# Kernel tuning notes

Measured on AMD Instinct MI355X. Metric: run time of the kernel, lower is better.

## Reference

```python
import jax, jax.numpy as jnp
import numpy as np

SR = 44100.0
MIN_GAIN, MAX_GAIN = -48.0, 12.0
MIN_EQ, MAX_EQ = -15.0, 15.0
MIN_CTS, MAX_CTS = -20.0, 10.0
# Freeverb (JUCE Reverb, as used by pedalboard.Reverb) tunings @ 44.1 kHz
COMB_T = [1116, 1188, 1277, 1356, 1422, 1491, 1557, 1617]
AP_T = [556, 441, 341, 225]
COMB_OFF = [0]
for _L in COMB_T:
    COMB_OFF.append(COMB_OFF[-1] + _L)
AP_OFF = [0]
for _L in AP_T:
    AP_OFF.append(AP_OFF[-1] + _L)


def restore(x, lo, hi):
    # inverse of normalize-to-(0,1)
    return x * (hi - lo) + lo


def first_order(fc, kind):
    # bilinear-transform 1st-order HP/LP (pedalboard High/LowpassFilter are 1st order)
    K = jnp.tan(np.pi * fc / SR)
    a1 = (K - 1.0) / (K + 1.0)
    z = jnp.zeros_like(fc)
    if kind == "hp":
        b0 = 1.0 / (1.0 + K)
        b = jnp.stack([b0, -b0, z], -1)
    else:
        b0 = K / (1.0 + K)
        b = jnp.stack([b0, b0, z], -1)
    a = jnp.stack([jnp.ones_like(fc), a1, z], -1)
    return b, a


def shelf(fc, gain_db, high):
    # RBJ cookbook shelf, Q = 1/sqrt(2)
    A = 10.0 ** (gain_db / 40.0)
    w = 2.0 * np.pi * fc / SR
    cw = jnp.cos(w)
    alpha = jnp.sin(w) * (np.sqrt(2.0) / 2.0)
    sq = 2.0 * jnp.sqrt(A) * alpha
    s = 1.0 if high else -1.0
    b0 = A * ((A + 1.0) + s * (A - 1.0) * cw + sq)
    b1 = -2.0 * s * A * ((A - 1.0) + s * (A + 1.0) * cw)
    b2 = A * ((A + 1.0) + s * (A - 1.0) * cw - sq)
    a0 = (A + 1.0) - s * (A - 1.0) * cw + sq
    a1 = 2.0 * s * ((A - 1.0) - s * (A + 1.0) * cw)
    a2 = (A + 1.0) - s * (A - 1.0) * cw - sq
    return jnp.stack([b0, b1, b2], -1), jnp.stack([a0, a1, a2], -1)


def peak(fc, gain_db, q):
    # RBJ cookbook peaking EQ
    A = 10.0 ** (gain_db / 40.0)
    w = 2.0 * np.pi * fc / SR
    cw = jnp.cos(w)
    alpha = jnp.sin(w) / (2.0 * q)
    b = jnp.stack([1.0 + alpha * A, -2.0 * cw, 1.0 - alpha * A], -1)
    a = jnp.stack([1.0 + alpha / A, -2.0 * cw, 1.0 - alpha / A], -1)
    return b, a


def cascade_biquads(x, B, A):
    # x: [N, T]; B, A: [N, 6, 3]. DF2T cascade of 6 sections via one scan.
    B = B / A[..., :1]
    A = A / A[..., :1]
    n_sec = B.shape[1]

    def step(z, xt):  # z: [N, 6, 2], xt: [N]
        s = xt
        zn = []
        for k in range(n_sec):
            y = B[:, k, 0] * s + z[:, k, 0]
            z1 = B[:, k, 1] * s - A[:, k, 1] * y + z[:, k, 1]
            z2 = B[:, k, 2] * s - A[:, k, 2] * y
            zn.append(jnp.stack([z1, z2], -1))
            s = y
        return jnp.stack(zn, 1), s

    z0 = jnp.zeros((x.shape[0], n_sec, 2), x.dtype)
    _, y = jax.lax.scan(step, z0, x.T)
    return y.T


def compressor(x, thr_db, ratio, att_ms, rel_ms):
    # feed-forward compressor, dB-domain gain computer + one-pole attack/release
    a_att = jnp.exp(-1.0 / (att_ms * 1e-3 * SR))  # [N]
    a_rel = jnp.exp(-1.0 / (rel_ms * 1e-3 * SR))
    lvl = 20.0 * jnp.log10(jnp.abs(x) + 1e-6)  # [N, T]
    tgt = jnp.minimum(0.0, (thr_db[:, None] - lvl) * (1.0 - 1.0 / ratio[:, None]))

    def step(g, t):  # g, t: [N] gain reduction in dB (<= 0)
        coef = jnp.where(t < g, a_att, a_rel)
        g = coef * g + (1.0 - coef) * t
        return g, g

    _, g = jax.lax.scan(step, jnp.zeros(x.shape[0], x.dtype), tgt.T)
    return x * 10.0 ** (g.T / 20.0)


def freeverb(x, room, damp01, wet, dry, width):
    # JUCE/Freeverb mono: 8 parallel damped combs -> 4 series allpasses
    fb = room * 0.28 + 0.7
    damp = damp01 * 0.4
    wet1 = 3.0 * wet * 0.5 * (1.0 + width)
    dryg = 2.0 * dry
    N = x.shape[0]
    CL, AL = COMB_OFF[-1], AP_OFF[-1]

    def step(carry, xt):
        cb, ab, st, t = carry
        inp = xt * 0.015
        acc = jnp.zeros_like(xt)
        st_new = []
        for k in range(8):
            idx = COMB_OFF[k] + t % COMB_T[k]
            out = cb[:, idx]
            s = out * (1.0 - damp) + st[:, k] * damp
            cb = cb.at[:, idx].set(inp + s * fb)
            st_new.append(s)
            acc = acc + out
        for k in range(4):
            idx = AP_OFF[k] + t % AP_T[k]
            buf = ab[:, idx]
            ab = ab.at[:, idx].set(acc + buf * 0.5)
            acc = buf - acc
        y = acc * wet1 + xt * dryg
        return (cb, ab, jnp.stack(st_new, 1), t + 1), y

    carry0 = (jnp.zeros((N, CL), x.dtype), jnp.zeros((N, AL), x.dtype),
              jnp.zeros((N, 8), x.dtype), jnp.int32(0))
    _, y = jax.lax.scan(step, carry0, x.T)
    return y.T


def _forward(x, p):
    bs, nt, T = x.shape
    N = bs * nt
    xf = x.reshape(N, T)
    pf = p.reshape(N, 24)

    gain_in = restore(pf[:, 0], MIN_GAIN, MAX_GAIN)
    xf = xf * (10.0 ** (gain_in / 20.0))[:, None]

    hp_fc = restore(pf[:, 1], 0.0, 350.0)
    lp_fc = restore(pf[:, 2], 3000.0, 22000.0)
    hs_fc = restore(pf[:, 3], 1500.0, 16000.0)
    hs_g = restore(pf[:, 4], MIN_EQ, MAX_EQ)
    ls_fc = restore(pf[:, 5], 30.0, 450.0)
    ls_g = restore(pf[:, 6], MIN_EQ, MAX_EQ)
    mh_fc = restore(pf[:, 7], 600.0, 7000.0)
    mh_g = restore(pf[:, 8], MIN_EQ, MAX_EQ)
    mh_q = restore(pf[:, 9], 0.5, 3.0)
    ml_fc = restore(pf[:, 10], 200.0, 2500.0)
    ml_g = restore(pf[:, 11], MIN_EQ, MAX_EQ)
    ml_q = restore(pf[:, 12], 0.5, 3.0)
    c_thr = restore(pf[:, 13], MIN_CTS, MAX_CTS)
    c_rat = restore(pf[:, 14], 1.0, 20.0)
    c_att = restore(pf[:, 15], 1.0, 30.0)
    c_rel = restore(pf[:, 16], 100.0, 4000.0)

    coefs = [first_order(hp_fc, "hp"), first_order(lp_fc, "lp"),
             shelf(hs_fc, hs_g, True), shelf(ls_fc, ls_g, False),
             peak(mh_fc, mh_g, mh_q), peak(ml_fc, ml_g, ml_q)]
    B = jnp.stack([c[0] for c in coefs], 1)  # [N, 6, 3]
    A = jnp.stack([c[1] for c in coefs], 1)
    xf = cascade_biquads(xf, B, A)
    xf = compressor(xf, c_thr, c_rat, c_att, c_rel)
    xf = freeverb(xf, pf[:, 17], pf[:, 18], pf[:, 19], pf[:, 20], pf[:, 21])

    gain_out = restore(pf[:, 22], MIN_GAIN, MAX_GAIN)
    xf = xf * (10.0 ** (gain_out / 20.0))[:, None]

    pan = restore(pf[:, 23], 0.3, 0.7)
    theta = pan * (np.pi / 2.0)
    pang = jnp.stack([jnp.cos(theta), jnp.sin(theta)], -1).reshape(bs, nt, 2)
    y = jnp.einsum("bnt,bnc->bct", xf.reshape(bs, nt, T), pang)

    p_out = jnp.stack([gain_in, hp_fc, lp_fc, hs_fc, hs_g, ls_fc, ls_g,
                       mh_fc, mh_g, mh_q, ml_fc, ml_g, ml_q,
                       c_thr, c_rat, c_att, c_rel,
                       pf[:, 17], pf[:, 18], pf[:, 19], pf[:, 20], pf[:, 21],
                       gain_out, pan], -1).reshape(bs, nt, 24)
    return y, p_out


_forward_jit = jax.jit(_forward)


def setup_inputs() -> dict:
    key = jax.random.key(0)
    k1, k2 = jax.random.split(key)
    x = 0.1 * jax.random.normal(k1, (4, 8, 65536), dtype=jnp.float32)
    p = jax.random.uniform(k2, (4, 8, 24), dtype=jnp.float32)
    return {"x": x, "p": p}


def reference(x, p):
    return _forward_jit(x, p)
```

## Files before the change

kernel.cpp:

```cpp
#include <hip/hip_runtime.h>
#include <math.h>

#define T 65536
#define NCH 32
#define LCHUNK 512
#define CCHUNK 128
#define SB 256
#define NBLK 256

#define OFS_A  0
#define OFS_B1 2097152
#define OFS_I  4194304
#define OFS_P  7340032
#define OFS_M  7342080
#define OFS_V  7346688
#define OFS_Z  7395840


__device__ void norm_store(double b0,double b1,double b2,double a0,double a1,double a2,
                           double* B, double* A1, double* A2, int k){
  B[k*3+0]=b0/a0; B[k*3+1]=b1/a0; B[k*3+2]=b2/a0; A1[k]=a1/a0; A2[k]=a2/a0;
}

__device__ void shelf_coefs(double fc, double g, double s, double* B, double* A1, double* A2, int k){
  double A  = pow(10.0, g/40.0);
  double w  = 2.0*3.14159265358979323846*fc/44100.0;
  double cw = cos(w);
  double al = sin(w)*0.70710678118654752;
  double sq = 2.0*sqrt(A)*al;
  double b0 = A*((A+1.0) + s*(A-1.0)*cw + sq);
  double b1 = -2.0*s*A*((A-1.0) + s*(A+1.0)*cw);
  double b2 = A*((A+1.0) + s*(A-1.0)*cw - sq);
  double a0 = (A+1.0) - s*(A-1.0)*cw + sq;
  double a1 = 2.0*s*((A-1.0) - s*(A+1.0)*cw);
  double a2 = (A+1.0) - s*(A-1.0)*cw - sq;
  norm_store(b0,b1,b2,a0,a1,a2,B,A1,A2,k);
}

__device__ void peak_coefs(double fc, double g, double q, double* B, double* A1, double* A2, int k){
  double A  = pow(10.0, g/40.0);
  double w  = 2.0*3.14159265358979323846*fc/44100.0;
  double cw = cos(w);
  double al = sin(w)/(2.0*q);
  norm_store(1.0+al*A, -2.0*cw, 1.0-al*A, 1.0+al/A, -2.0*cw, 1.0-al/A, B,A1,A2,k);
}

__global__ void k_params(const float* __restrict__ p, float* __restrict__ ws, float* __restrict__ pout){
  int ch = threadIdx.x;
  if (ch >= NCH) return;
  const float* pf = p + ch*24;
  float f[24];
  #pragma unroll
  for (int j=0;j<24;j++) f[j]=pf[j];

  double gain_in = (double)f[0]*60.0 - 48.0;
  double hp_fc  = (double)f[1]*350.0;
  double lp_fc  = (double)f[2]*19000.0 + 3000.0;
  double hs_fc  = (double)f[3]*14500.0 + 1500.0;
  double hs_g   = (double)f[4]*30.0 - 15.0;
  double ls_fc  = (double)f[5]*420.0 + 30.0;
  double ls_g   = (double)f[6]*30.0 - 15.0;
  double mh_fc  = (double)f[7]*6400.0 + 600.0;
  double mh_g   = (double)f[8]*30.0 - 15.0;
  double mh_q   = (double)f[9]*2.5 + 0.5;
  double ml_fc  = (double)f[10]*2300.0 + 200.0;
  double ml_g   = (double)f[11]*30.0 - 15.0;
  double ml_q   = (double)f[12]*2.5 + 0.5;
  double c_thr  = (double)f[13]*30.0 - 20.0;
  double c_rat  = (double)f[14]*19.0 + 1.0;
  double c_att  = (double)f[15]*29.0 + 1.0;
  double c_rel  = (double)f[16]*3900.0 + 100.0;
  double gain_out=(double)f[22]*60.0 - 48.0;
  double pan    = (double)f[23]*0.4 + 0.3;

  double B[18], A1[6], A2[6];
  { double K = tan(3.14159265358979323846*hp_fc/44100.0);
    double a1=(K-1.0)/(K+1.0), b0=1.0/(1.0+K);
    B[0]=b0; B[1]=-b0; B[2]=0.0; A1[0]=a1; A2[0]=0.0; }
  { double K = tan(3.14159265358979323846*lp_fc/44100.0);
    double a1=(K-1.0)/(K+1.0), b0=K/(1.0+K);
    B[3]=b0; B[4]=b0; B[5]=0.0; A1[1]=a1; A2[1]=0.0; }
  shelf_coefs(hs_fc, hs_g,  1.0, B, A1, A2, 2);
  shelf_coefs(ls_fc, ls_g, -1.0, B, A1, A2, 3);
  peak_coefs (mh_fc, mh_g, mh_q, B, A1, A2, 4);
  peak_coefs (ml_fc, ml_g, ml_q, B, A1, A2, 5);

  double gin = pow(10.0, gain_in/20.0);
  B[0]*=gin; B[1]*=gin; B[2]*=gin;

  float* Pc = ws + OFS_P + ch*64;
  #pragma unroll
  for (int k=0;k<6;k++){
    Pc[k]    = (float)B[k*3+0];
    Pc[6+k]  = (float)B[k*3+1];
    Pc[12+k] = (float)B[k*3+2];
    Pc[18+k] = (float)A1[k];
    Pc[24+k] = (float)A2[k];
  }
  Pc[30] = (float)c_thr;
  Pc[31] = (float)(1.0 - 1.0/c_rat);
  Pc[32] = (float)exp(-1.0/(c_att*0.001*44100.0));
  Pc[33] = (float)exp(-1.0/(c_rel*0.001*44100.0));
  double fb   = (double)f[17]*0.28 + 0.7;
  double damp = (double)f[18]*0.4;
  double wet1 = 3.0*(double)f[19]*0.5*(1.0+(double)f[21]);
  double dryg = 2.0*(double)f[20];
  double gout = pow(10.0, gain_out/20.0);
  Pc[34] = (float)fb;
  Pc[35] = (float)damp;
  Pc[36] = (float)(wet1*gout);
  Pc[37] = (float)(dryg*gout/0.015);
  Pc[38] = (float)cos(pan*1.57079632679489662);
  Pc[39] = (float)sin(pan*1.57079632679489662);

  float* po = pout + ch*24;
  po[0]=(float)gain_in; po[1]=(float)hp_fc; po[2]=(float)lp_fc; po[3]=(float)hs_fc;
  po[4]=(float)hs_g; po[5]=(float)ls_fc; po[6]=(float)ls_g; po[7]=(float)mh_fc;
  po[8]=(float)mh_g; po[9]=(float)mh_q; po[10]=(float)ml_fc; po[11]=(float)ml_g;
  po[12]=(float)ml_q; po[13]=(float)c_thr; po[14]=(float)c_rat; po[15]=(float)c_att;
  po[16]=(float)c_rel; po[17]=f[17]; po[18]=f[18]; po[19]=f[19]; po[20]=f[20];
  po[21]=f[21]; po[22]=(float)gain_out; po[23]=(float)pan;
}


__device__ __forceinline__ float bq_step(const float* b0, const float* b1, const float* b2,
                                         const float* a1, const float* a2,
                                         float* z1, float* z2, float s){
  #pragma unroll
  for (int k=0;k<6;k++){
    float y = fmaf(b0[k], s, z1[k]);
    z1[k] = fmaf(b1[k], s, fmaf(-a1[k], y, z2[k]));
    z2[k] = fmaf(b2[k], s, -a2[k]*y);
    s = y;
  }
  return s;
}

__device__ __forceinline__ void load_coefs(const float* Pc, float* b0, float* b1, float* b2,
                                           float* a1, float* a2){
  #pragma unroll
  for (int k=0;k<6;k++){
    b0[k]=Pc[k]; b1[k]=Pc[6+k]; b2[k]=Pc[12+k]; a1[k]=Pc[18+k]; a2[k]=Pc[24+k];
  }
}

__global__ void k_chunk1(const float* __restrict__ x, float* __restrict__ ws){
  int tg = blockIdx.x*64 + threadIdx.x;
  int ch = tg / 140, sub = tg % 140;
  if (ch >= NCH) return;
  const float* Pc = ws + OFS_P + ch*64;
  float b0[6],b1[6],b2[6],a1[6],a2[6];
  load_coefs(Pc,b0,b1,b2,a1,a2);
  float z1[6]={0,0,0,0,0,0}, z2[6]={0,0,0,0,0,0};

  if (sub < CCHUNK){
    const float4* xp = (const float4*)(x + ch*T + sub*LCHUNK);
    for (int j=0;j<LCHUNK/4;j++){
      float4 v = xp[j];
      bq_step(b0,b1,b2,a1,a2,z1,z2,v.x);
      bq_step(b0,b1,b2,a1,a2,z1,z2,v.y);
      bq_step(b0,b1,b2,a1,a2,z1,z2,v.z);
      bq_step(b0,b1,b2,a1,a2,z1,z2,v.w);
    }
    float* vo = ws + OFS_V + (ch*CCHUNK + sub)*12;
    #pragma unroll
    for (int k=0;k<6;k++){ vo[2*k]=z1[k]; vo[2*k+1]=z2[k]; }
  } else {
    int j = sub - CCHUNK;
    if ((j & 1)==0) z1[j>>1]=1.0f; else z2[j>>1]=1.0f;
    for (int t=0;t<LCHUNK;t++) bq_step(b0,b1,b2,a1,a2,z1,z2,0.0f);
    float* mo = ws + OFS_M + ch*144 + j*12;
    #pragma unroll
    for (int k=0;k<6;k++){ mo[2*k]=z1[k]; mo[2*k+1]=z2[k]; }
  }
}

__global__ void k_chunk2(float* __restrict__ ws){
  int ch = threadIdx.x;
  if (ch >= NCH) return;
  const float* M = ws + OFS_M + ch*144;
  const float* V = ws + OFS_V + ch*CCHUNK*12;
  float*       Z = ws + OFS_Z + ch*CCHUNK*12;
  float z[12];
  #pragma unroll
  for (int i=0;i<12;i++) z[i]=0.0f;
  for (int c=0;c<CCHUNK;c++){
    #pragma unroll
    for (int i=0;i<12;i++) Z[c*12+i]=z[i];
    float zn[12];
    #pragma unroll
    for (int i=0;i<12;i++) zn[i]=V[c*12+i];
    #pragma unroll
    for (int j=0;j<12;j++){
      float zj = z[j];
      #pragma unroll
      for (int i=0;i<12;i++) zn[i] = fmaf(M[j*12+i], zj, zn[i]);
    }
    #pragma unroll
    for (int i=0;i<12;i++) z[i]=zn[i];
  }
}

__global__ void k_chunk3(const float* __restrict__ x, float* __restrict__ ws){
  int tg = blockIdx.x*64 + threadIdx.x;
  int ch = tg >> 7, c = tg & (CCHUNK-1);
  const float* Pc = ws + OFS_P + ch*64;
  float b0[6],b1[6],b2[6],a1[6],a2[6];
  load_coefs(Pc,b0,b1,b2,a1,a2);
  float thr = Pc[30], rt = Pc[31];
  float aA = Pc[32], aR = Pc[33];
  float kA = 1.0f - aA, kR = 1.0f - aR;
  const float* Zi = ws + OFS_Z + (ch*CCHUNK + c)*12;
  float z1[6], z2[6];
  #pragma unroll
  for (int k=0;k<6;k++){ z1[k]=Zi[2*k]; z2[k]=Zi[2*k+1]; }
  const float4* xp = (const float4*)(x + ch*T + c*LCHUNK);
  float4* Ao  = (float4*)(ws + OFS_A  + (size_t)ch*T + c*LCHUNK);
  float4* B1o = (float4*)(ws + OFS_B1 + (size_t)ch*T + c*LCHUNK);
  float*  Ig  = ws + OFS_I + (size_t)ch*98304;

  for (int gg=0; gg<64; gg++){
    float4 v0 = xp[2*gg], v1 = xp[2*gg+1];
    float ya[8], Tv[8];
    ya[0]=bq_step(b0,b1,b2,a1,a2,z1,z2,v0.x);
    ya[1]=bq_step(b0,b1,b2,a1,a2,z1,z2,v0.y);
    ya[2]=bq_step(b0,b1,b2,a1,a2,z1,z2,v0.z);
    ya[3]=bq_step(b0,b1,b2,a1,a2,z1,z2,v0.w);
    ya[4]=bq_step(b0,b1,b2,a1,a2,z1,z2,v1.x);
    ya[5]=bq_step(b0,b1,b2,a1,a2,z1,z2,v1.y);
    ya[6]=bq_step(b0,b1,b2,a1,a2,z1,z2,v1.z);
    ya[7]=bq_step(b0,b1,b2,a1,a2,z1,z2,v1.w);
    #pragma unroll
    for (int s=0;s<8;s++)
      Tv[s] = fminf(0.0f, (thr - 6.0205999132796239f*log2f(fabsf(ya[s])+1e-6f))*rt);
    Ao[2*gg]   = make_float4(ya[0],ya[1],ya[2],ya[3]);
    Ao[2*gg+1] = make_float4(ya[4],ya[5],ya[6],ya[7]);
    B1o[2*gg]   = make_float4(Tv[0],Tv[1],Tv[2],Tv[3]);
    B1o[2*gg+1] = make_float4(Tv[4],Tv[5],Tv[6],Tv[7]);
    float bb[9];
    bb[0] = kR*Tv[0]; bb[1] = kA*Tv[0];
    #pragma unroll
    for (int s=1;s<8;s++){
      float bA = kA*Tv[s], bR = kR*Tv[s];
      bb[s+1] = fmaf(aA, bb[s], bA);
      #pragma unroll
      for (int j=7;j>=1;j--){
        if (j<=s) bb[j] = fminf(fmaf(aA, bb[j-1], bA), fmaf(aR, bb[j], bR));
      }
      bb[0] = fmaf(aR, bb[0], bR);
    }
    int G = c*64 + gg;
    float* ig = Ig + (G>>5)*384 + (G&31)*12;
    *(float4*)(ig)   = make_float4(bb[0],bb[1],bb[2],bb[3]);
    *(float4*)(ig+4) = make_float4(bb[4],bb[5],bb[6],bb[7]);
    *(float4*)(ig+8) = make_float4(bb[8],0.0f,0.0f,0.0f);
  }
}


__global__ __launch_bounds__(320) void k_verb(float* __restrict__ ws){
  const int LC[8] = {1116,1188,1277,1356,1422,1491,1557,1617};
  const int COFF[8] = {0,1116,2304,3581,4937,6359,7850,9407};
  const int LA[4] = {556,441,341,225};
  const int AOFF[4] = {0,556,997,1338};
  int ch = blockIdx.x, tid = threadIdx.x;
  __shared__ float cb[11024];
  __shared__ float ab[1563];
  __shared__ float cH[8][266];
  __shared__ float xts[256];
  __shared__ float B1st[2][256];
  __shared__ float IldS[384];
  __shared__ float gB[2][32];
  __shared__ float xfer[32];
  const float* Pc = ws + OFS_P + ch*64;
  float fb = Pc[34], damp = Pc[35], wet1 = Pc[36], dryk = Pc[37];
  float aA = Pc[32], aR = Pc[33];
  float kA = 1.0f - aA, kR = 1.0f - aR;
  float omd = 1.0f - damp;
  float* Aio = ws + OFS_A + (size_t)ch*T;
  const float* B1c = ws + OFS_B1 + (size_t)ch*T;
  const float* IG  = ws + OFS_I + (size_t)ch*98304;
  for (int i=tid;i<11024;i+=320) cb[i]=0.0f;
  for (int i=tid;i<1563;i+=320)  ab[i]=0.0f;
  for (int i=tid;i<8*266;i+=320) ((float*)cH)[i]=0.0f;
  bool scanw = (tid >= 256);
  int sl = tid - 256;
  float w[10];
  { float pw = 1.0f;
    #pragma unroll
    for (int d=0;d<10;d++){ w[d]=pw; pw*=damp; } }
  float sj[9];
  { float pA = 1.0f;
    #pragma unroll
    for (int j=0;j<9;j++){ sj[j]=pA; pA*=aA; }
    float pR = 1.0f;
    #pragma unroll
    for (int j=8;j>=0;j--){ sj[j]*=pR; pR*=aR; } }
  int cbb[8] = {0,0,0,0,0,0,0,0};
  int abb[4] = {0,0,0,0};
  float gcarry = 0.0f;
  float4 iR0, iR1, bR;
  float xv = 0.0f;

  if (scanw){
    const float4* isrc = (const float4*)(IG);
    float4* idst = (float4*)IldS;
    idst[sl] = isrc[sl];
    if (sl < 32) idst[64+sl] = isrc[64+sl];
    iR0 = isrc[96+sl];
    if (sl < 32) iR1 = isrc[96+64+sl];
    const float4* bsrc = (const float4*)(B1c);
    ((float4*)B1st[0])[sl] = bsrc[sl];
    ((float4*)B1st[1])[sl] = bsrc[64+sl];
  }
  if (tid < 256) xv = Aio[tid];
  __syncthreads();
  if (tid == 256){
    float g = 0.0f;
    for (int m=0;m<32;m++){
      gB[0][m] = g;
      const float* Ip = &IldS[m*12];
      float f0=fmaf(sj[0],g,Ip[0]), f1=fmaf(sj[1],g,Ip[1]), f2=fmaf(sj[2],g,Ip[2]);
      float f3=fmaf(sj[3],g,Ip[3]), f4=fmaf(sj[4],g,Ip[4]), f5=fmaf(sj[5],g,Ip[5]);
      float f6=fmaf(sj[6],g,Ip[6]), f7=fmaf(sj[7],g,Ip[7]), f8=fmaf(sj[8],g,Ip[8]);
      g = fminf(fminf(fminf(f0,f1),fminf(f2,f3)),
                fminf(fminf(f4,f5),fminf(fminf(f6,f7),f8)));
    }
    gcarry = g;
  }
  __syncthreads();

  for (int i=0;i<NBLK;i++){
    int t0 = i<<8;
    float xt = 0.0f, acc = 0.0f, a = 0.0f;
    if (tid < 256){
      int m = tid>>3, r = tid&7;
      float g = gB[i&1][m];
      const float* Bl = B1st[i&1] + (m<<3);
      #pragma unroll
      for (int s=0;s<8;s++){
        if (s<=r){
          float tt = Bl[s];
          g = fminf(fmaf(aA,g,kA*tt), fmaf(aR,g,kR*tt));
        }
      }
      xt = xv * exp2f(g*0.16609640474436813f) * 0.015f;
      xts[tid] = xt;
      #pragma unroll
      for (int k=0;k<8;k++){
        int idx = cbb[k]+tid; if (idx>=LC[k]) idx-=LC[k];
        float o = cb[COFF[k]+idx];
        cH[k][10+tid] = omd*o;
        acc += o;
      }
    } else if (i+1 < NBLK){
      float4* idst = (float4*)IldS;
      idst[sl] = iR0;
      if (sl < 32) idst[64+sl] = iR1;
      if (i >= 1) ((float4*)B1st[(i+1)&1])[sl] = bR;
    }
    __syncthreads();
    if (tid < 256){
      if (i+1 < NBLK) xv = Aio[t0+256+tid];
      #pragma unroll
      for (int k=0;k<8;k++){
        float s = 0.0f;
        #pragma unroll
        for (int d=0;d<10;d++) s = fmaf(w[d], cH[k][10+tid-d], s);
        int idx = cbb[k]+tid; if (idx>=LC[k]) idx-=LC[k];
        cb[COFF[k]+idx] = fmaf(fb, s, xt);
      }
      a = acc;
      #pragma unroll
      for (int j=0;j<3;j++){
        int idx = abb[j]+tid; if (idx>=LA[j]) idx-=LA[j];
        float bv = ab[AOFF[j]+idx];
        ab[AOFF[j]+idx] = fmaf(0.5f, bv, a);
        a = bv - a;
      }
      if (tid >= 225) xfer[tid-225] = a;
    } else {
      if (i+2 < NBLK){
        const float4* isrc = (const float4*)(IG + (size_t)(i+2)*384);
        iR0 = isrc[sl];
        if (sl < 32) iR1 = isrc[64+sl];
        const float4* bsrc = (const float4*)(B1c + (size_t)(i+2)*SB);
        bR = bsrc[sl];
      }
      if (tid == 256 && i+1 < NBLK){
        int p = (i+1)&1;
        float g = gcarry;
        #pragma unroll 4
        for (int m=0;m<32;m++){
          gB[p][m] = g;
          const float* Ip = &IldS[m*12];
          float f0=fmaf(sj[0],g,Ip[0]), f1=fmaf(sj[1],g,Ip[1]), f2=fmaf(sj[2],g,Ip[2]);
          float f3=fmaf(sj[3],g,Ip[3]), f4=fmaf(sj[4],g,Ip[4]), f5=fmaf(sj[5],g,Ip[5]);
          float f6=fmaf(sj[6],g,Ip[6]), f7=fmaf(sj[7],g,Ip[7]), f8=fmaf(sj[8],g,Ip[8]);
          g = fminf(fminf(fminf(f0,f1),fminf(f2,f3)),
                    fminf(fminf(f4,f5),fminf(fminf(f6,f7),f8)));
        }
        gcarry = g;
      }
    }
    __syncthreads();
    if (tid < 225){
      int idx = abb[3]+tid; if (idx>=225) idx-=225;
      float bv = ab[AOFF[3]+idx];
      float b  = fmaf(0.5f, bv, a);
      float y  = bv - a;
      Aio[t0+tid] = fmaf(y, wet1, xts[tid]*dryk);
      if (tid < 31){
        float a2 = xfer[tid];
        float y2 = b - a2;
        ab[AOFF[3]+idx] = fmaf(0.5f, b, a2);
        Aio[t0+225+tid] = fmaf(y2, wet1, xts[225+tid]*dryk);
      } else {
        ab[AOFF[3]+idx] = b;
      }
    } else if (tid >= 232 && tid < 312){
      int q = tid-232; int k = q/10, d = q%10;
      cH[k][d] = cH[k][256+d];
    }
    #pragma unroll
    for (int k=0;k<8;k++){ cbb[k]+=SB; if (cbb[k]>=LC[k]) cbb[k]-=LC[k]; }
    #pragma unroll
    for (int j=0;j<4;j++){
      abb[j]+=SB;
      if (abb[j]>=LA[j]) abb[j]-=LA[j];
      if (abb[j]>=LA[j]) abb[j]-=LA[j];
    }
    __syncthreads();
  }
}


__global__ void k_mix(const float* __restrict__ ws, float* __restrict__ out){
  int id = blockIdx.x*256 + threadIdx.x;
  int t = id & (T-1), b = id >> 16;
  const float* Av = ws + OFS_A + (size_t)b*8*T + t;
  const float* P = ws + OFS_P;
  float s0=0.0f, s1=0.0f;
  #pragma unroll
  for (int n=0;n<8;n++){
    float v = Av[(size_t)n*T];
    int ch = b*8+n;
    s0 = fmaf(v, P[ch*64+38], s0);
    s1 = fmaf(v, P[ch*64+39], s1);
  }
  out[b*2*T + t]     = s0;
  out[b*2*T + T + t] = s1;
}

extern "C" void kernel_launch(void* const* d_in, const int* in_sizes, int n_in,
                              void* d_out, int out_size, void* d_ws, size_t ws_size,
                              hipStream_t stream) {
  const float* x = (const float*)d_in[0];
  const float* p = (const float*)d_in[1];
  float* out = (float*)d_out;
  float* ws  = (float*)d_ws;

  k_params<<<1, 64, 0, stream>>>(p, ws, out + 4*2*T);
  k_chunk1<<<70, 64, 0, stream>>>(x, ws);
  k_chunk2<<<1, 64, 0, stream>>>(ws);
  k_chunk3<<<64, 64, 0, stream>>>(x, ws);
  k_verb  <<<NCH, 320, 0, stream>>>(ws);
  k_mix   <<<(4*T)/256, 256, 0, stream>>>(ws, out);
}
```

Baseline: 996.7 us.

## Compute compressor block summaries in verb kernel and drop one barrier per block

Result: slower. 1.098 ms (+10.1%).

```diff
diff --git a/kernel.cpp b/kernel.cpp
--- a/kernel.cpp
+++ b/kernel.cpp
@@ -10,11 +10,10 @@
 
 #define OFS_A  0
 #define OFS_B1 2097152
-#define OFS_I  4194304
-#define OFS_P  7340032
-#define OFS_M  7342080
-#define OFS_V  7346688
-#define OFS_Z  7395840
+#define OFS_P  4194304
+#define OFS_M  4196352
+#define OFS_V  4200960
+#define OFS_Z  4250112
 
 
 __device__ void norm_store(double b0,double b1,double b2,double a0,double a1,double a2,
@@ -208,8 +207,6 @@
   float b0[6],b1[6],b2[6],a1[6],a2[6];
   load_coefs(Pc,b0,b1,b2,a1,a2);
   float thr = Pc[30], rt = Pc[31];
-  float aA = Pc[32], aR = Pc[33];
-  float kA = 1.0f - aA, kR = 1.0f - aR;
   const float* Zi = ws + OFS_Z + (ch*CCHUNK + c)*12;
   float z1[6], z2[6];
   #pragma unroll
@@ -217,43 +214,17 @@
   const float4* xp = (const float4*)(x + ch*T + c*LCHUNK);
   float4* Ao  = (float4*)(ws + OFS_A  + (size_t)ch*T + c*LCHUNK);
   float4* B1o = (float4*)(ws + OFS_B1 + (size_t)ch*T + c*LCHUNK);
-  float*  Ig  = ws + OFS_I + (size_t)ch*98304;
-
-  for (int gg=0; gg<64; gg++){
-    float4 v0 = xp[2*gg], v1 = xp[2*gg+1];
-    float ya[8], Tv[8];
-    ya[0]=bq_step(b0,b1,b2,a1,a2,z1,z2,v0.x);
-    ya[1]=bq_step(b0,b1,b2,a1,a2,z1,z2,v0.y);
-    ya[2]=bq_step(b0,b1,b2,a1,a2,z1,z2,v0.z);
-    ya[3]=bq_step(b0,b1,b2,a1,a2,z1,z2,v0.w);
-    ya[4]=bq_step(b0,b1,b2,a1,a2,z1,z2,v1.x);
-    ya[5]=bq_step(b0,b1,b2,a1,a2,z1,z2,v1.y);
-    ya[6]=bq_step(b0,b1,b2,a1,a2,z1,z2,v1.z);
-    ya[7]=bq_step(b0,b1,b2,a1,a2,z1,z2,v1.w);
-    #pragma unroll
-    for (int s=0;s<8;s++)
-      Tv[s] = fminf(0.0f, (thr - 6.0205999132796239f*log2f(fabsf(ya[s])+1e-6f))*rt);
-    Ao[2*gg]   = make_float4(ya[0],ya[1],ya[2],ya[3]);
-    Ao[2*gg+1] = make_float4(ya[4],ya[5],ya[6],ya[7]);
-    B1o[2*gg]   = make_float4(Tv[0],Tv[1],Tv[2],Tv[3]);
-    B1o[2*gg+1] = make_float4(Tv[4],Tv[5],Tv[6],Tv[7]);
-    float bb[9];
-    bb[0] = kR*Tv[0]; bb[1] = kA*Tv[0];
-    #pragma unroll
-    for (int s=1;s<8;s++){
-      float bA = kA*Tv[s], bR = kR*Tv[s];
-      bb[s+1] = fmaf(aA, bb[s], bA);
-      #pragma unroll
-      for (int j=7;j>=1;j--){
-        if (j<=s) bb[j] = fminf(fmaf(aA, bb[j-1], bA), fmaf(aR, bb[j], bR));
-      }
-      bb[0] = fmaf(aR, bb[0], bR);
-    }
-    int G = c*64 + gg;
-    float* ig = Ig + (G>>5)*384 + (G&31)*12;
-    *(float4*)(ig)   = make_float4(bb[0],bb[1],bb[2],bb[3]);
-    *(float4*)(ig+4) = make_float4(bb[4],bb[5],bb[6],bb[7]);
-    *(float4*)(ig+8) = make_float4(bb[8],0.0f,0.0f,0.0f);
+  for (int j=0;j<LCHUNK/4;j++){
+    float4 v = xp[j], ya, tb;
+    ya.x = bq_step(b0,b1,b2,a1,a2,z1,z2,v.x);
+    ya.y = bq_step(b0,b1,b2,a1,a2,z1,z2,v.y);
+    ya.z = bq_step(b0,b1,b2,a1,a2,z1,z2,v.z);
+    ya.w = bq_step(b0,b1,b2,a1,a2,z1,z2,v.w);
+    tb.x = fminf(0.0f, (thr - 6.0205999132796239f*log2f(fabsf(ya.x)+1e-6f))*rt);
+    tb.y = fminf(0.0f, (thr - 6.0205999132796239f*log2f(fabsf(ya.y)+1e-6f))*rt);
+    tb.z = fminf(0.0f, (thr - 6.0205999132796239f*log2f(fabsf(ya.z)+1e-6f))*rt);
+    tb.w = fminf(0.0f, (thr - 6.0205999132796239f*log2f(fabsf(ya.w)+1e-6f))*rt);
+    Ao[j]=ya; B1o[j]=tb;
   }
 }
 
@@ -266,12 +237,12 @@
   int ch = blockIdx.x, tid = threadIdx.x;
   __shared__ float cb[11024];
   __shared__ float ab[1563];
-  __shared__ float cH[8][266];
+  __shared__ float cH[2][8][266];
   __shared__ float xts[256];
+  __shared__ float accS[256];
   __shared__ float B1st[2][256];
-  __shared__ float IldS[384];
+  __shared__ float Ild[384];
   __shared__ float gB[2][32];
-  __shared__ float xfer[32];
   const float* Pc = ws + OFS_P + ch*64;
   float fb = Pc[34], damp = Pc[35], wet1 = Pc[36], dryk = Pc[37];
   float aA = Pc[32], aR = Pc[33];
@@ -279,10 +250,9 @@
   float omd = 1.0f - damp;
   float* Aio = ws + OFS_A + (size_t)ch*T;
   const float* B1c = ws + OFS_B1 + (size_t)ch*T;
-  const float* IG  = ws + OFS_I + (size_t)ch*98304;
   for (int i=tid;i<11024;i+=320) cb[i]=0.0f;
   for (int i=tid;i<1563;i+=320)  ab[i]=0.0f;
-  for (int i=tid;i<8*266;i+=320) ((float*)cH)[i]=0.0f;
+  for (int i=tid;i<2*8*266;i+=320) ((float*)cH)[i]=0.0f;
   bool scanw = (tid >= 256);
   int sl = tid - 256;
   float w[10];
@@ -299,19 +269,33 @@
   int cbb[8] = {0,0,0,0,0,0,0,0};
   int abb[4] = {0,0,0,0};
   float gcarry = 0.0f;
-  float4 iR0, iR1, bR;
+  float4 bR;
   float xv = 0.0f;
 
   if (scanw){
-    const float4* isrc = (const float4*)(IG);
-    float4* idst = (float4*)IldS;
-    idst[sl] = isrc[sl];
-    if (sl < 32) idst[64+sl] = isrc[64+sl];
-    iR0 = isrc[96+sl];
-    if (sl < 32) iR1 = isrc[96+64+sl];
     const float4* bsrc = (const float4*)(B1c);
     ((float4*)B1st[0])[sl] = bsrc[sl];
     ((float4*)B1st[1])[sl] = bsrc[64+sl];
+    if (sl < 32){
+      const float* Bv = B1st[0] + (sl<<3);
+      float Tv[8];
+      #pragma unroll
+      for (int j=0;j<8;j++) Tv[j]=Bv[j];
+      float bb[9];
+      bb[0]=kR*Tv[0]; bb[1]=kA*Tv[0];
+      #pragma unroll
+      for (int s=1;s<8;s++){
+        float bA=kA*Tv[s], bRv=kR*Tv[s];
+        bb[s+1]=fmaf(aA, bb[s], bA);
+        #pragma unroll
+        for (int j=7;j>=1;j--) if (j<=s) bb[j]=fminf(fmaf(aA,bb[j-1],bA), fmaf(aR,bb[j],bRv));
+        bb[0]=fmaf(aR,bb[0],bRv);
+      }
+      float* ig=&Ild[sl*12];
+      *(float4*)(ig)   = make_float4(bb[0],bb[1],bb[2],bb[3]);
+      *(float4*)(ig+4) = make_float4(bb[4],bb[5],bb[6],bb[7]);
+      ig[8]=bb[8];
+    }
   }
   if (tid < 256) xv = Aio[tid];
   __syncthreads();
@@ -319,7 +303,7 @@
     float g = 0.0f;
     for (int m=0;m<32;m++){
       gB[0][m] = g;
-      const float* Ip = &IldS[m*12];
+      const float* Ip = &Ild[m*12];
       float f0=fmaf(sj[0],g,Ip[0]), f1=fmaf(sj[1],g,Ip[1]), f2=fmaf(sj[2],g,Ip[2]);
       float f3=fmaf(sj[3],g,Ip[3]), f4=fmaf(sj[4],g,Ip[4]), f5=fmaf(sj[5],g,Ip[5]);
       float f6=fmaf(sj[6],g,Ip[6]), f7=fmaf(sj[7],g,Ip[7]), f8=fmaf(sj[8],g,Ip[8]);
@@ -332,11 +316,12 @@
 
   for (int i=0;i<NBLK;i++){
     int t0 = i<<8;
-    float xt = 0.0f, acc = 0.0f, a = 0.0f;
+    int p = i & 1;
+    float xt = 0.0f, acc = 0.0f;
     if (tid < 256){
       int m = tid>>3, r = tid&7;
-      float g = gB[i&1][m];
-      const float* Bl = B1st[i&1] + (m<<3);
+      float g = gB[p][m];
+      const float* Bl = B1st[p] + (m<<3);
       #pragma unroll
       for (int s=0;s<8;s++){
         if (s<=r){
@@ -350,14 +335,34 @@
       for (int k=0;k<8;k++){
         int idx = cbb[k]+tid; if (idx>=LC[k]) idx-=LC[k];
         float o = cb[COFF[k]+idx];
-        cH[k][10+tid] = omd*o;
+        float cv = omd*o;
+        cH[p][k][10+tid] = cv;
+        if (tid >= 246) cH[p^1][k][tid-246] = cv;
         acc += o;
       }
-    } else if (i+1 < NBLK){
-      float4* idst = (float4*)IldS;
-      idst[sl] = iR0;
-      if (sl < 32) idst[64+sl] = iR1;
-      if (i >= 1) ((float4*)B1st[(i+1)&1])[sl] = bR;
+      accS[tid] = acc;
+    } else {
+      if (i >= 1 && i+1 < NBLK) ((float4*)B1st[(i+1)&1])[sl] = bR;
+      if (i+1 < NBLK && sl < 32){
+        const float* Bv = B1st[(i+1)&1] + (sl<<3);
+        float Tv[8];
+        #pragma unroll
+        for (int j=0;j<8;j++) Tv[j]=Bv[j];
+        float bb[9];
+        bb[0]=kR*Tv[0]; bb[1]=kA*Tv[0];
+        #pragma unroll
+        for (int s=1;s<8;s++){
+          float bA=kA*Tv[s], bRv=kR*Tv[s];
+          bb[s+1]=fmaf(aA, bb[s], bA);
+          #pragma unroll
+          for (int j=7;j>=1;j--) if (j<=s) bb[j]=fminf(fmaf(aA,bb[j-1],bA), fmaf(aR,bb[j],bRv));
+          bb[0]=fmaf(aR,bb[0],bRv);
+        }
+        float* ig=&Ild[sl*12];
+        *(float4*)(ig)   = make_float4(bb[0],bb[1],bb[2],bb[3]);
+        *(float4*)(ig+4) = make_float4(bb[4],bb[5],bb[6],bb[7]);
+        ig[8]=bb[8];
+      }
     }
     __syncthreads();
     if (tid < 256){
@@ -366,11 +371,11 @@
       for (int k=0;k<8;k++){
         float s = 0.0f;
         #pragma unroll
-        for (int d=0;d<10;d++) s = fmaf(w[d], cH[k][10+tid-d], s);
+        for (int d=0;d<10;d++) s = fmaf(w[d], cH[p][k][10+tid-d], s);
         int idx = cbb[k]+tid; if (idx>=LC[k]) idx-=LC[k];
         cb[COFF[k]+idx] = fmaf(fb, s, xt);
       }
-      a = acc;
+      float a = acc;
       #pragma unroll
       for (int j=0;j<3;j++){
         int idx = abb[j]+tid; if (idx>=LA[j]) idx-=LA[j];
@@ -378,22 +383,45 @@
         ab[AOFF[j]+idx] = fmaf(0.5f, bv, a);
         a = bv - a;
       }
-      if (tid >= 225) xfer[tid-225] = a;
+      bool dual = (tid < 31);
+      float a2 = 0.0f, xt2 = 0.0f;
+      if (dual){
+        a2 = accS[tid+225];
+        xt2 = xts[tid+225];
+        #pragma unroll
+        for (int j=0;j<3;j++){
+          int idx = abb[j]+tid+225;
+          if (idx>=LA[j]) idx-=LA[j];
+          if (idx>=LA[j]) idx-=LA[j];
+          float bv = ab[AOFF[j]+idx];
+          ab[AOFF[j]+idx] = fmaf(0.5f, bv, a2);
+          a2 = bv - a2;
+        }
+      }
+      if (tid < 225){
+        int idx = abb[3]+tid; if (idx>=225) idx-=225;
+        float bv = ab[AOFF[3]+idx];
+        float b  = fmaf(0.5f, bv, a);
+        float y  = bv - a;
+        Aio[t0+tid] = fmaf(y, wet1, xt*dryk);
+        if (dual){
+          float y2 = b - a2;
+          ab[AOFF[3]+idx] = fmaf(0.5f, b, a2);
+          Aio[t0+225+tid] = fmaf(y2, wet1, xt2*dryk);
+        } else {
+          ab[AOFF[3]+idx] = b;
+        }
+      }
     } else {
-      if (i+2 < NBLK){
-        const float4* isrc = (const float4*)(IG + (size_t)(i+2)*384);
-        iR0 = isrc[sl];
-        if (sl < 32) iR1 = isrc[64+sl];
-        const float4* bsrc = (const float4*)(B1c + (size_t)(i+2)*SB);
-        bR = bsrc[sl];
-      }
+      if (i+2 < NBLK)
+        bR = ((const float4*)(B1c + (size_t)(i+2)*SB))[sl];
       if (tid == 256 && i+1 < NBLK){
-        int p = (i+1)&1;
+        int q = (i+1)&1;
         float g = gcarry;
         #pragma unroll 4
         for (int m=0;m<32;m++){
-          gB[p][m] = g;
-          const float* Ip = &IldS[m*12];
+          gB[q][m] = g;
+          const float* Ip = &Ild[m*12];
           float f0=fmaf(sj[0],g,Ip[0]), f1=fmaf(sj[1],g,Ip[1]), f2=fmaf(sj[2],g,Ip[2]);
           float f3=fmaf(sj[3],g,Ip[3]), f4=fmaf(sj[4],g,Ip[4]), f5=fmaf(sj[5],g,Ip[5]);
           float f6=fmaf(sj[6],g,Ip[6]), f7=fmaf(sj[7],g,Ip[7]), f8=fmaf(sj[8],g,Ip[8]);
@@ -403,25 +431,6 @@
         gcarry = g;
       }
     }
-    __syncthreads();
-    if (tid < 225){
-      int idx = abb[3]+tid; if (idx>=225) idx-=225;
-      float bv = ab[AOFF[3]+idx];
-      float b  = fmaf(0.5f, bv, a);
-      float y  = bv - a;
-      Aio[t0+tid] = fmaf(y, wet1, xts[tid]*dryk);
-      if (tid < 31){
-        float a2 = xfer[tid];
-        float y2 = b - a2;
-        ab[AOFF[3]+idx] = fmaf(0.5f, b, a2);
-        Aio[t0+225+tid] = fmaf(y2, wet1, xts[225+tid]*dryk);
-      } else {
-        ab[AOFF[3]+idx] = b;
-      }
-    } else if (tid >= 232 && tid < 312){
-      int q = tid-232; int k = q/10, d = q%10;
-      cH[k][d] = cH[k][256+d];
-    }
     #pragma unroll
     for (int k=0;k<8;k++){ cbb[k]+=SB; if (cbb[k]>=LC[k]) cbb[k]-=LC[k]; }
     #pragma unroll
```
